# Optimization experiments

Hardware: AMD Instinct MI355X
Metric: run time of the kernel (lower is better)

The kernel has to match this reference:

```python
import jax, jax.numpy as jnp
import numpy as np
import math

EPS = 1e-5

def layernorm(x, w, b):
    mu = jnp.mean(x, axis=-1, keepdims=True)
    var = jnp.mean((x - mu) ** 2, axis=-1, keepdims=True)
    return (x - mu) / jnp.sqrt(var + EPS) * w + b

def pos_encoding(L, D):
    pos = jnp.arange(L, dtype=jnp.float32)[:, None]
    div = jnp.exp(jnp.arange(0, D, 2, dtype=jnp.float32) * (-math.log(10000.0) / D))
    pe = jnp.zeros((L, D), dtype=jnp.float32)
    pe = pe.at[:, 0::2].set(jnp.sin(pos * div))
    pe = pe.at[:, 1::2].set(jnp.cos(pos * div))
    return pe

def ssm_block(x, nw, nb, A, iw, ib, ow, ob):
    # x: [B,L,D]
    z = layernorm(x, nw, nb)
    proj = jnp.einsum('bld,ed->ble', z, iw) + ib  # [B,L,2D]
    u, g = jnp.split(proj, 2, axis=-1)
    g = jax.nn.sigmoid(g)
    u_t = jnp.swapaxes(u, 0, 1)  # [L,B,D]
    g_t = jnp.swapaxes(g, 0, 1)
    h0 = jnp.zeros(x.shape[::2], dtype=x.dtype)  # [B,D]
    def step(h, ug):
        ut, gt = ug
        h = gt * h + (1.0 - gt) * jnp.tanh(A * h + ut)
        return h, h
    _, hs = jax.lax.scan(step, h0, (u_t, g_t))  # hs: [L,B,D]
    out = jnp.einsum('lbd,ed->ble', hs, ow).swapaxes(0, 1).swapaxes(0, 1)
    out = jnp.einsum('lbd,ed->ble', hs, ow) + ob
    return x + out

def mha(x, qkv_w, qkv_b, ao_w, ao_b, nhead):
    B, L, D = x.shape
    dh = D // nhead
    qkv = jnp.einsum('bld,ed->ble', x, qkv_w) + qkv_b  # [B,L,3D]
    q, k, v = jnp.split(qkv, 3, axis=-1)
    def heads(t):
        return t.reshape(B, L, nhead, dh).transpose(0, 2, 1, 3)  # [B,H,L,dh]
    q, k, v = heads(q), heads(k), heads(v)
    scores = jnp.einsum('bhqd,bhkd->bhqk', q, k) / jnp.sqrt(jnp.asarray(dh, x.dtype))
    attn = jax.nn.softmax(scores, axis=-1)
    out = jnp.einsum('bhqk,bhkd->bhqd', attn, v)
    out = out.transpose(0, 2, 1, 3).reshape(B, L, D)
    return jnp.einsum('bld,ed->ble', out, ao_w) + ao_b

def encoder_layer(x, l1w, l1b, l2w, l2b, qkv_w, qkv_b, ao_w, ao_b, f1w, f1b, f2w, f2b, nhead):
    # norm_first pre-LN encoder layer, relu FFN, no dropout (eval)
    x = x + mha(layernorm(x, l1w, l1b), qkv_w, qkv_b, ao_w, ao_b, nhead)
    h = layernorm(x, l2w, l2b)
    h = jax.nn.relu(jnp.einsum('bld,fd->blf', h, f1w) + f1b)
    h = jnp.einsum('blf,df->bld', h, f2w) + f2b
    return x + h

def setup_inputs() -> dict:
    key = jax.random.key(0)
    ks = jax.random.split(key, 16)
    B, L, F, D, S, T = 8, 2048, 64, 128, 2, 2
    s = 0.05
    inp = {
        'x': jax.random.normal(ks[0], (B, L, F), jnp.float32),
        'in_w': jax.random.normal(ks[1], (D, F), jnp.float32) * s,
        'in_b': jnp.zeros((D,), jnp.float32),
        'ssm_norm_w': jnp.ones((S, D), jnp.float32),
        'ssm_norm_b': jnp.zeros((S, D), jnp.float32),
        'ssm_A': jax.random.normal(ks[2], (S, D), jnp.float32) * 0.1,
        'ssm_in_w': jax.random.normal(ks[3], (S, 2 * D, D), jnp.float32) * s,
        'ssm_in_b': jnp.zeros((S, 2 * D), jnp.float32),
        'ssm_out_w': jax.random.normal(ks[4], (S, D, D), jnp.float32) * s,
        'ssm_out_b': jnp.zeros((S, D), jnp.float32),
        'ln1_w': jnp.ones((T, D), jnp.float32),
        'ln1_b': jnp.zeros((T, D), jnp.float32),
        'ln2_w': jnp.ones((T, D), jnp.float32),
        'ln2_b': jnp.zeros((T, D), jnp.float32),
        'qkv_w': jax.random.normal(ks[5], (T, 3 * D, D), jnp.float32) * s,
        'qkv_b': jnp.zeros((T, 3 * D), jnp.float32),
        'ao_w': jax.random.normal(ks[6], (T, D, D), jnp.float32) * s,
        'ao_b': jnp.zeros((T, D), jnp.float32),
        'ff1_w': jax.random.normal(ks[7], (T, 4 * D, D), jnp.float32) * s,
        'ff1_b': jnp.zeros((T, 4 * D), jnp.float32),
        'ff2_w': jax.random.normal(ks[8], (T, D, 4 * D), jnp.float32) * s,
        'ff2_b': jnp.zeros((T, D), jnp.float32),
        'hln_w': jnp.ones((D,), jnp.float32),
        'hln_b': jnp.zeros((D,), jnp.float32),
        'h1_w': jax.random.normal(ks[9], (D, D), jnp.float32) * s,
        'h1_b': jnp.zeros((D,), jnp.float32),
        'h2_w': jax.random.normal(ks[10], (1, D), jnp.float32) * s,
        'h2_b': jnp.zeros((1,), jnp.float32),
    }
    return inp

NHEAD = 4

def reference(x, in_w, in_b, ssm_norm_w, ssm_norm_b, ssm_A, ssm_in_w, ssm_in_b,
              ssm_out_w, ssm_out_b, ln1_w, ln1_b, ln2_w, ln2_b, qkv_w, qkv_b,
              ao_w, ao_b, ff1_w, ff1_b, ff2_w, ff2_b, hln_w, hln_b, h1_w, h1_b,
              h2_w, h2_b):
    B, L, _ = x.shape
    D = in_w.shape[0]
    h = jnp.einsum('blf,df->bld', x, in_w) + in_b
    h = h + pos_encoding(L, D)[None]
    for i in range(ssm_A.shape[0]):
        h = ssm_block(h, ssm_norm_w[i], ssm_norm_b[i], ssm_A[i],
                      ssm_in_w[i], ssm_in_b[i], ssm_out_w[i], ssm_out_b[i])
    for i in range(ln1_w.shape[0]):
        h = encoder_layer(h, ln1_w[i], ln1_b[i], ln2_w[i], ln2_b[i],
                          qkv_w[i], qkv_b[i], ao_w[i], ao_b[i],
                          ff1_w[i], ff1_b[i], ff2_w[i], ff2_b[i], NHEAD)
    pooled = 0.5 * h[:, -1, :] + 0.5 * jnp.mean(h, axis=1)  # [B,D]
    p = layernorm(pooled, hln_w, hln_b)
    p = jax.nn.gelu(p @ h1_w.T + h1_b, approximate=False)
    return p @ h2_w.T + h2_b  # [B,1]
```

## Files before the change

kernel.cpp:

```cpp
#include <hip/hip_runtime.h>
#include <hip/hip_bf16.h>
#include <math.h>

#define L_SEQ 2048
#define D_MODEL 128
#define N_ROWS 16384
#define LOG2E 1.4426950408889634f

typedef __attribute__((ext_vector_type(8))) short bf16x8;
typedef __attribute__((ext_vector_type(4))) short short4v;
typedef __attribute__((ext_vector_type(4))) float f32x4;
typedef __attribute__((ext_vector_type(4))) unsigned uint4v;

__device__ __forceinline__ short f2bf(float x)
{
    __hip_bfloat16 b = __float2bfloat16(x);
    return *reinterpret_cast<short*>(&b);
}
__device__ __forceinline__ short f2bf_fast(float x)
{
    unsigned u = __builtin_bit_cast(unsigned, x);
    return (short)((u + 0x8000u) >> 16);
}
__device__ __forceinline__ unsigned cvt_pk_bf16(float lo, float hi)
{
    unsigned r;
    asm("v_cvt_pk_bf16_f32 %0, %1, %2" : "=v"(r) : "v"(lo), "v"(hi));
    return r;
}
__device__ __forceinline__ float bf2f(short s)
{
    unsigned u = ((unsigned)(unsigned short)s) << 16;
    return __builtin_bit_cast(float, u);
}
__device__ __forceinline__ short f2h(float x)
{
    _Float16 h = (_Float16)x;
    return (short)__builtin_bit_cast(unsigned short, h);
}
__device__ __forceinline__ float h2f(short s)
{
    _Float16 h = __builtin_bit_cast(_Float16, (unsigned short)s);
    return (float)h;
}

__global__ __launch_bounds__(256) void convert_kernel(
    const float* __restrict__ x,    const float* __restrict__ inw,
    const float* __restrict__ ssmi, const float* __restrict__ ssmo,
    const float* __restrict__ qkvw, const float* __restrict__ aow,
    const float* __restrict__ f1w,  const float* __restrict__ f2w,
    short* __restrict__ xb, short* __restrict__ wb)
{
    int it = blockIdx.x * 256 + threadIdx.x;
    const float* src; short* dst; int off;
    if      (it < 131072) { src = x;    dst = xb;          off = it; }
    else if (it < 132096) { src = inw;  dst = wb;          off = it - 131072; }
    else if (it < 140288) { src = ssmi; dst = wb + 8192;   off = it - 132096; }
    else if (it < 144384) { src = ssmo; dst = wb + 73728;  off = it - 140288; }
    else if (it < 156672) { src = qkvw; dst = wb + 106496; off = it - 144384; }
    else if (it < 160768) { src = aow;  dst = wb + 204800; off = it - 156672; }
    else if (it < 177152) { src = f1w;  dst = wb + 237568; off = it - 160768; }
    else                  { src = f2w;  dst = wb + 368640; off = it - 177152; }
    off <<= 3;
    float4 v0 = *(const float4*)(src + off);
    float4 v1 = *(const float4*)(src + off + 4);
    bf16x8 p = {f2bf(v0.x), f2bf(v0.y), f2bf(v0.z), f2bf(v0.w),
                f2bf(v1.x), f2bf(v1.y), f2bf(v1.z), f2bf(v1.w)};
    *(bf16x8*)(dst + off) = p;
}

template <int FUSE, int RED>
__global__ __launch_bounds__(256) void gemm_ln(const short* __restrict__ A,
                                               const short* __restrict__ W,
                                               const float* __restrict__ bias,
                                               const float* __restrict__ lnw,
                                               const float* __restrict__ lnb,
                                               float* __restrict__ bh,
                                               short* __restrict__ lnout,
                                               int K,
                                               const float* __restrict__ pO,
                                               const float* __restrict__ prs)
{
    __shared__ __align__(16) short As[32][72];
    __shared__ __align__(16) short Bs[128][72];
    __shared__ float2 red[2][32];

    const int tid  = threadIdx.x;
    const int wave = tid >> 6;
    const int lane = tid & 63;
    const int m    = lane & 15;
    const int quad = lane >> 4;
    const int rh   = wave & 1;
    const int ch   = wave >> 1;
    const int n0   = blockIdx.x * 32;

    const int arow = tid >> 3, acol = (tid & 7) << 3;
    const int brow = tid >> 1, bcol = (tid & 1) << 5;

    const short* Ap = A + (size_t)(n0 + arow) * K + acol;
    const short* Wp = W + (size_t)brow * K + bcol;

    f32x4 acc[4];
#pragma unroll
    for (int i = 0; i < 4; ++i) acc[i] = (f32x4){0.f, 0.f, 0.f, 0.f};

    bf16x8 a0;
    float4 ra0, ra1, rb0, rb1;
    float inva = 0.f;
    if (RED) {
        int row = n0 + arow;
        int hh  = acol >> 5;
        float rsv = prs[(size_t)hh * N_ROWS + row] + prs[(size_t)(4 + hh) * N_ROWS + row];
        inva = 1.f / rsv;
        const float* p0 = pO + (size_t)row * 128 + acol;
        const float* p1 = p0 + (size_t)N_ROWS * 128;
        ra0 = *(const float4*)p0;
        ra1 = *(const float4*)(p0 + 4);
        rb0 = *(const float4*)p1;
        rb1 = *(const float4*)(p1 + 4);
    } else {
        a0 = *(const bf16x8*)Ap;
    }
    bf16x8 b0 = *(const bf16x8*)Wp;
    bf16x8 b1 = *(const bf16x8*)(Wp + 8);
    bf16x8 b2 = *(const bf16x8*)(Wp + 16);
    bf16x8 b3 = *(const bf16x8*)(Wp + 24);

    for (int k0 = 0; k0 < K; k0 += 64) {
        if (RED) {
            uint4v pk;
            pk.x = cvt_pk_bf16((ra0.x + rb0.x) * inva, (ra0.y + rb0.y) * inva);
            pk.y = cvt_pk_bf16((ra0.z + rb0.z) * inva, (ra0.w + rb0.w) * inva);
            pk.z = cvt_pk_bf16((ra1.x + rb1.x) * inva, (ra1.y + rb1.y) * inva);
            pk.w = cvt_pk_bf16((ra1.z + rb1.z) * inva, (ra1.w + rb1.w) * inva);
            *(bf16x8*)&As[arow][acol] = __builtin_bit_cast(bf16x8, pk);
        } else {
            *(bf16x8*)&As[arow][acol] = a0;
        }
        *(bf16x8*)&Bs[brow][bcol]      = b0;
        *(bf16x8*)&Bs[brow][bcol + 8]  = b1;
        *(bf16x8*)&Bs[brow][bcol + 16] = b2;
        *(bf16x8*)&Bs[brow][bcol + 24] = b3;
        __syncthreads();
        if (k0 + 64 < K) {
            if (RED) {
                int row = n0 + arow;
                int col = k0 + 64 + acol;
                int hh  = col >> 5;
                float rsv = prs[(size_t)hh * N_ROWS + row] + prs[(size_t)(4 + hh) * N_ROWS + row];
                inva = 1.f / rsv;
                const float* p0 = pO + (size_t)row * 128 + col;
                const float* p1 = p0 + (size_t)N_ROWS * 128;
                ra0 = *(const float4*)p0;
                ra1 = *(const float4*)(p0 + 4);
                rb0 = *(const float4*)p1;
                rb1 = *(const float4*)(p1 + 4);
            } else {
                a0 = *(const bf16x8*)(Ap + k0 + 64);
            }
            b0 = *(const bf16x8*)(Wp + k0 + 64);
            b1 = *(const bf16x8*)(Wp + k0 + 72);
            b2 = *(const bf16x8*)(Wp + k0 + 80);
            b3 = *(const bf16x8*)(Wp + k0 + 88);
        }
#pragma unroll
        for (int ks = 0; ks < 2; ++ks) {
            bf16x8 af = *(const bf16x8*)&As[(rh << 4) + m][(ks << 5) + (quad << 3)];
#pragma unroll
            for (int nt = 0; nt < 4; ++nt) {
                bf16x8 bfr = *(const bf16x8*)&Bs[(ch << 6) + (nt << 4) + m][(ks << 5) + (quad << 3)];
                acc[nt] = __builtin_amdgcn_mfma_f32_16x16x32_bf16(af, bfr, acc[nt], 0, 0, 0);
            }
        }
        __syncthreads();
    }

#pragma unroll
    for (int nt = 0; nt < 4; ++nt) {
        int col = (ch << 6) + (nt << 4) + m;
        float bv = bias[col];
        float fr = 0.f;
        if (FUSE == 0)
            fr = __expf((float)(col & ~1) * (-0.07195578415606394f));
#pragma unroll
        for (int r = 0; r < 4; ++r) {
            int row = n0 + (rh << 4) + (quad << 2) + r;
            float t = acc[nt][r] + bv;
            if (FUSE == 0) {
                float ang = (float)(row & (L_SEQ - 1)) * fr;
                t += (col & 1) ? cosf(ang) : sinf(ang);
            } else {
                t += bh[(size_t)row * 128 + col];
            }
            acc[nt][r] = t;
            bh[(size_t)row * 128 + col] = t;
        }
    }

    if (FUSE < 2) {
        float wv[4], bvn[4];
#pragma unroll
        for (int nt = 0; nt < 4; ++nt) {
            wv[nt]  = lnw[(ch << 6) + (nt << 4) + m];
            bvn[nt] = lnb[(ch << 6) + (nt << 4) + m];
        }
        float s1[4], s2[4];
#pragma unroll
        for (int r = 0; r < 4; ++r) {
            float s = 0.f, q = 0.f;
#pragma unroll
            for (int nt = 0; nt < 4; ++nt) {
                float t = acc[nt][r];
                s += t;
                q = fmaf(t, t, q);
            }
            s += __shfl_xor(s, 1);  q += __shfl_xor(q, 1);
            s += __shfl_xor(s, 2);  q += __shfl_xor(q, 2);
            s += __shfl_xor(s, 4);  q += __shfl_xor(q, 4);
            s += __shfl_xor(s, 8);  q += __shfl_xor(q, 8);
            s1[r] = s; s2[r] = q;
            if (m == 0) red[ch][(rh << 4) + (quad << 2) + r] = make_float2(s, q);
        }
        __syncthreads();
#pragma unroll
        for (int r = 0; r < 4; ++r) {
            float2 o = red[ch ^ 1][(rh << 4) + (quad << 2) + r];
            float ts = s1[r] + o.x;
            float tq = s2[r] + o.y;
            float mean = ts * (1.f / 128.f);
            float var  = tq * (1.f / 128.f) - mean * mean;
            float inv  = rsqrtf(var + 1e-5f);
            int row = n0 + (rh << 4) + (quad << 2) + r;
#pragma unroll
            for (int nt = 0; nt < 4; ++nt) {
                int col = (ch << 6) + (nt << 4) + m;
                lnout[(size_t)row * 128 + col] =
                    f2bf((acc[nt][r] - mean) * inv * wv[nt] + bvn[nt]);
            }
        }
    }
}

enum { EPI_BF_RELU = 0, EPI_QKV = 1, EPI_SCAN_T = 2 };

template <int EPI>
__global__ __launch_bounds__(256) void gemm_bf(const short* __restrict__ A,
                                               const short* __restrict__ W,
                                               const float* __restrict__ bias,
                                               short* __restrict__ outb,
                                               short* __restrict__ outv,
                                               int K, int E)
{
    __shared__ __align__(16) short As[64][136];
    __shared__ __align__(16) short Bs[64][136];

    const int tid  = threadIdx.x;
    const int wave = tid >> 6;
    const int lane = tid & 63;
    const int m    = lane & 15;
    const int quad = lane >> 4;

    const int n0 = blockIdx.y * 64;
    const int e0 = blockIdx.x * 64;

    const int srow = tid >> 2;
    const int scol = (tid & 3) << 5;

    const short* Ap = A + (size_t)(n0 + srow) * K + scol;
    const short* Wp = W + (size_t)(e0 + srow) * K + scol;

    bf16x8 a0 = *(const bf16x8*)(Ap);
    bf16x8 a1 = *(const bf16x8*)(Ap + 8);
    bf16x8 a2 = *(const bf16x8*)(Ap + 16);
    bf16x8 a3 = *(const bf16x8*)(Ap + 24);
    bf16x8 w0 = *(const bf16x8*)(Wp);
    bf16x8 w1 = *(const bf16x8*)(Wp + 8);
    bf16x8 w2 = *(const bf16x8*)(Wp + 16);
    bf16x8 w3 = *(const bf16x8*)(Wp + 24);
    *(bf16x8*)&As[srow][scol]      = a0;
    *(bf16x8*)&As[srow][scol + 8]  = a1;
    *(bf16x8*)&As[srow][scol + 16] = a2;
    *(bf16x8*)&As[srow][scol + 24] = a3;
    *(bf16x8*)&Bs[srow][scol]      = w0;
    *(bf16x8*)&Bs[srow][scol + 8]  = w1;
    *(bf16x8*)&Bs[srow][scol + 16] = w2;
    *(bf16x8*)&Bs[srow][scol + 24] = w3;
    __syncthreads();

    f32x4 acc[4];
#pragma unroll
    for (int i = 0; i < 4; ++i) acc[i] = (f32x4){0.f, 0.f, 0.f, 0.f};

#pragma unroll
    for (int ks = 0; ks < 4; ++ks) {
        bf16x8 af = *(const bf16x8*)&As[(wave << 4) + m][(ks << 5) + (quad << 3)];
#pragma unroll
        for (int nt = 0; nt < 4; ++nt) {
            bf16x8 bfr = *(const bf16x8*)&Bs[(nt << 4) + m][(ks << 5) + (quad << 3)];
            acc[nt] = __builtin_amdgcn_mfma_f32_16x16x32_bf16(af, bfr, acc[nt], 0, 0, 0);
        }
    }

    if (EPI == EPI_QKV) {
        const float QSC = 0.17677669529663687f * LOG2E;
        if (e0 < 256) {
            short* dst = (e0 < 128) ? outb : (outb + 2097152);
            int cbase = (e0 < 128) ? e0 : (e0 - 128);
#pragma unroll
            for (int nt = 0; nt < 4; ++nt) {
                int col = cbase + (nt << 4) + m;
                float bv = bias[e0 + (nt << 4) + m];
#pragma unroll
                for (int r = 0; r < 4; ++r) {
                    int row = n0 + (wave << 4) + (quad << 2) + r;
                    float v = acc[nt][r] + bv;
                    if (e0 < 128) v *= QSC;
                    dst[(size_t)row * 128 + col] = f2bf(v);
                }
            }
        } else {
            int bb_ = n0 >> 11;
            int l0  = (n0 & (L_SEQ - 1)) + (wave << 4) + (quad << 2);
#pragma unroll
            for (int nt = 0; nt < 4; ++nt) {
                int c  = (e0 - 256) + (nt << 4) + m;
                int hh = c >> 5, dd = c & 31;
                float bv = bias[e0 + (nt << 4) + m];
                short4v pk;
#pragma unroll
                for (int r = 0; r < 4; ++r) pk[r] = f2bf(acc[nt][r] + bv);
                *(short4v*)&outv[(size_t)((bb_ * 4 + hh) * 32 + dd) * L_SEQ + l0] = pk;
            }
        }
    } else if (EPI == EPI_SCAN_T) {
        int bb_ = n0 >> 11;
        int l0  = (n0 & (L_SEQ - 1)) + (wave << 4) + (quad << 2);
#pragma unroll
        for (int nt = 0; nt < 4; ++nt) {
            int col = e0 + (nt << 4) + m;
            float bv = bias[col];
            short4v pk;
            if (e0 < 128) {
#pragma unroll
                for (int r = 0; r < 4; ++r)
                    pk[r] = f2h((acc[nt][r] + bv) * (2.f * LOG2E));
            } else {
#pragma unroll
                for (int r = 0; r < 4; ++r) {
                    float gr = acc[nt][r] + bv;
                    float g = __builtin_amdgcn_rcpf(
                        1.f + __builtin_amdgcn_exp2f(-gr * LOG2E));
                    pk[r] = f2h(g);
                }
            }
            *(short4v*)&outb[(((size_t)(bb_ * 256 + col)) << 11) + l0] = pk;
        }
    } else {
#pragma unroll
        for (int nt = 0; nt < 4; ++nt) {
            int col = e0 + (nt << 4) + m;
            float bv = bias[col];
#pragma unroll
            for (int r = 0; r < 4; ++r) {
                int row = n0 + (wave << 4) + (quad << 2) + r;
                float v = fmaxf(acc[nt][r] + bv, 0.f);
                outb[(size_t)row * E + col] = f2bf(v);
            }
        }
    }
}

#define SCAN_WARM 128

__device__ __forceinline__ void scan8(float& h, bf16x8 u8, bf16x8 g8,
                                      float a2, short* __restrict__ ob, int l0)
{
#pragma unroll
    for (int i = 0; i < 8; ++i) {
        float u2 = h2f(u8[i]);
        float g  = h2f(g8[i]);
        float omg = 1.f - g;
        float m2  = -2.f * omg;
        float c0 = fmaf(g, h, omg);
        float e2 = __builtin_amdgcn_exp2f(fmaf(a2, h, u2));
        float r  = __builtin_amdgcn_rcpf(1.f + e2);
        h = fmaf(m2, r, c0);
        ob[(l0 + i) * D_MODEL] = f2bf(h);
    }
}

__device__ __forceinline__ void scan8_ns(float& h, bf16x8 u8, bf16x8 g8,
                                         float a2)
{
#pragma unroll
    for (int i = 0; i < 8; ++i) {
        float u2 = h2f(u8[i]);
        float g  = h2f(g8[i]);
        float omg = 1.f - g;
        float m2  = -2.f * omg;
        float c0 = fmaf(g, h, omg);
        float e2 = __builtin_amdgcn_exp2f(fmaf(a2, h, u2));
        float r  = __builtin_amdgcn_rcpf(1.f + e2);
        h = fmaf(m2, r, c0);
    }
}

__global__ __launch_bounds__(64) void scan_kernel(const short* __restrict__ pt,
                                                  const float* __restrict__ A,
                                                  short* __restrict__ hs)
{
    int blk = blockIdx.x;
    int c   = blk & 15;
    int bd  = blk >> 4;
    int b   = bd >> 1;
    int d   = ((bd & 1) << 6) + threadIdx.x;
    float a2 = 2.f * A[d] * LOG2E;
    const short* up = pt + (((size_t)(b * 256 + d)) << 11);
    const short* gp = up + (((size_t)128) << 11);
    short* ob = hs + ((size_t)(b << 11)) * D_MODEL + d;

    const int lw = c << 7;
    float h = 0.f;

    bf16x8 uA0, uA1, gA0, gA1;

    if (c > 0) {
        int l0 = lw - SCAN_WARM;
        uA0 = *(const bf16x8*)(up + l0);
        uA1 = *(const bf16x8*)(up + l0 + 8);
        gA0 = *(const bf16x8*)(gp + l0);
        gA1 = *(const bf16x8*)(gp + l0 + 8);
        for (int l = l0; l < lw; l += 32) {
            bf16x8 uB0 = *(const bf16x8*)(up + l + 16);
            bf16x8 uB1 = *(const bf16x8*)(up + l + 24);
            bf16x8 gB0 = *(const bf16x8*)(gp + l + 16);
            bf16x8 gB1 = *(const bf16x8*)(gp + l + 24);
            scan8_ns(h, uA0, gA0, a2);
            scan8_ns(h, uA1, gA1, a2);
            uA0 = *(const bf16x8*)(up + l + 32);
            uA1 = *(const bf16x8*)(up + l + 40);
            gA0 = *(const bf16x8*)(gp + l + 32);
            gA1 = *(const bf16x8*)(gp + l + 40);
            scan8_ns(h, uB0, gB0, a2);
            scan8_ns(h, uB1, gB1, a2);
        }
    } else {
        uA0 = *(const bf16x8*)(up);
        uA1 = *(const bf16x8*)(up + 8);
        gA0 = *(const bf16x8*)(gp);
        gA1 = *(const bf16x8*)(gp + 8);
    }

    for (int l = lw; l < lw + 128; l += 32) {
        bf16x8 uB0 = *(const bf16x8*)(up + l + 16);
        bf16x8 uB1 = *(const bf16x8*)(up + l + 24);
        bf16x8 gB0 = *(const bf16x8*)(gp + l + 16);
        bf16x8 gB1 = *(const bf16x8*)(gp + l + 24);
        scan8(h, uA0, gA0, a2, ob, l);
        scan8(h, uA1, gA1, a2, ob, l + 8);
        if (l + 32 < lw + 128) {
            uA0 = *(const bf16x8*)(up + l + 32);
            uA1 = *(const bf16x8*)(up + l + 40);
            gA0 = *(const bf16x8*)(gp + l + 32);
            gA1 = *(const bf16x8*)(gp + l + 40);
        }
        scan8(h, uB0, gB0, a2, ob, l + 16);
        scan8(h, uB1, gB1, a2, ob, l + 24);
    }
}

__global__ __launch_bounds__(256) void attn_kernel(const short* __restrict__ Qs,
                                                   const short* __restrict__ Ks,
                                                   const short* __restrict__ Vtg,
                                                   float* __restrict__ pO,
                                                   float* __restrict__ prs)
{
    __shared__ __align__(16) short Klds[2][64][40];
    __shared__ __align__(16) short Vlds[2][32][72];
    __shared__ __align__(16) short Plds[4][32][68];

    const int tid  = threadIdx.x;
    const int wave = tid >> 6;
    const int lane = tid & 63;
    const int m    = lane & 15;
    const int quad = lane >> 4;

    const int raw = blockIdx.x;
    const int bid = (raw & 7) * 128 + (raw >> 3);
    const int b    = bid >> 7;
    const int h    = (bid >> 5) & 3;
    const int qh   = bid & 31;
    const int q0   = (qh >> 1) << 7;
    const int half = qh & 1;
    const int kv0  = half << 10;

    const size_t qrow = (size_t)((b << 11) + q0 + (wave << 5) + m);
    bf16x8 qfA = *(const bf16x8*)&Qs[qrow * 128 + (h << 5) + (quad << 3)];
    bf16x8 qfB = *(const bf16x8*)&Qs[(qrow + 16) * 128 + (h << 5) + (quad << 3)];

    f32x4 O00 = {0.f,0.f,0.f,0.f}, O01 = {0.f,0.f,0.f,0.f};
    f32x4 O10 = {0.f,0.f,0.f,0.f}, O11 = {0.f,0.f,0.f,0.f};
    float rs0 = 0.f, rs1 = 0.f;

    const int krow = tid >> 2, dg = (tid & 3) << 3;
    const int vrow = tid >> 3, kg = (tid & 7) << 3;
    const short* kbase = Ks + ((size_t)((b << 11) + kv0) + krow) * 128 + (h << 5) + dg;
    const short* vbase = Vtg + ((size_t)((b << 2) + h) * 32 + vrow) * L_SEQ + kv0 + kg;

    bf16x8 kreg = *(const bf16x8*)kbase;
    bf16x8 vreg = *(const bf16x8*)vbase;
    *(bf16x8*)&Klds[0][krow][dg] = kreg;
    *(bf16x8*)&Vlds[0][vrow][kg] = vreg;
    __syncthreads();

    for (int kc = 0; kc < 16; ++kc) {
        const int cur = kc & 1;
        if (kc < 15) {
            kreg = *(const bf16x8*)(kbase + (size_t)((kc + 1) << 6) * 128);
            vreg = *(const bf16x8*)(vbase + ((kc + 1) << 6));
        }

#pragma unroll
        for (int kt = 0; kt < 4; ++kt) {
            bf16x8 kf = *(const bf16x8*)&Klds[cur][(kt << 4) + m][quad << 3];
            f32x4 S0 = __builtin_amdgcn_mfma_f32_16x16x32_bf16(
                kf, qfA, (f32x4){0.f, 0.f, 0.f, 0.f}, 0, 0, 0);
            f32x4 S1 = __builtin_amdgcn_mfma_f32_16x16x32_bf16(
                kf, qfB, (f32x4){0.f, 0.f, 0.f, 0.f}, 0, 0, 0);
            float a0 = __builtin_amdgcn_exp2f(S0[0]);
            float a1 = __builtin_amdgcn_exp2f(S0[1]);
            float a2 = __builtin_amdgcn_exp2f(S0[2]);
            float a3 = __builtin_amdgcn_exp2f(S0[3]);
            rs0 += a0 + a1 + a2 + a3;
            uint2 pkA;
            pkA.x = cvt_pk_bf16(a0, a1);
            pkA.y = cvt_pk_bf16(a2, a3);
            *(uint2*)&Plds[wave][m][(kt << 4) + (quad << 2)] = pkA;
            float b0 = __builtin_amdgcn_exp2f(S1[0]);
            float b1 = __builtin_amdgcn_exp2f(S1[1]);
            float b2 = __builtin_amdgcn_exp2f(S1[2]);
            float b3 = __builtin_amdgcn_exp2f(S1[3]);
            rs1 += b0 + b1 + b2 + b3;
            uint2 pkB;
            pkB.x = cvt_pk_bf16(b0, b1);
            pkB.y = cvt_pk_bf16(b2, b3);
            *(uint2*)&Plds[wave][16 + m][(kt << 4) + (quad << 2)] = pkB;
        }

#pragma unroll
        for (int kt2 = 0; kt2 < 2; ++kt2) {
            short4v aLo = *(const short4v*)&Plds[wave][m][(kt2 << 5) + (quad << 3)];
            short4v aHi = *(const short4v*)&Plds[wave][m][(kt2 << 5) + (quad << 3) + 4];
            bf16x8 pfA = {aLo[0], aLo[1], aLo[2], aLo[3],
                          aHi[0], aHi[1], aHi[2], aHi[3]};
            short4v bLo = *(const short4v*)&Plds[wave][16 + m][(kt2 << 5) + (quad << 3)];
            short4v bHi = *(const short4v*)&Plds[wave][16 + m][(kt2 << 5) + (quad << 3) + 4];
            bf16x8 pfB = {bLo[0], bLo[1], bLo[2], bLo[3],
                          bHi[0], bHi[1], bHi[2], bHi[3]};
            bf16x8 vf0 = *(const bf16x8*)&Vlds[cur][m][(kt2 << 5) + (quad << 3)];
            bf16x8 vf1 = *(const bf16x8*)&Vlds[cur][16 + m][(kt2 << 5) + (quad << 3)];
            O00 = __builtin_amdgcn_mfma_f32_16x16x32_bf16(pfA, vf0, O00, 0, 0, 0);
            O01 = __builtin_amdgcn_mfma_f32_16x16x32_bf16(pfA, vf1, O01, 0, 0, 0);
            O10 = __builtin_amdgcn_mfma_f32_16x16x32_bf16(pfB, vf0, O10, 0, 0, 0);
            O11 = __builtin_amdgcn_mfma_f32_16x16x32_bf16(pfB, vf1, O11, 0, 0, 0);
        }

        if (kc < 15) {
            *(bf16x8*)&Klds[cur ^ 1][krow][dg] = kreg;
            *(bf16x8*)&Vlds[cur ^ 1][vrow][kg] = vreg;
        }
        __syncthreads();
    }

    rs0 += __shfl_xor(rs0, 16);
    rs0 += __shfl_xor(rs0, 32);
    rs1 += __shfl_xor(rs1, 16);
    rs1 += __shfl_xor(rs1, 32);

    const int rowbase = (b << 11) + q0 + (wave << 5);
    if (quad == 0) {
        prs[(size_t)((half << 2) + h) * N_ROWS + rowbase + m]      = rs0;
        prs[(size_t)((half << 2) + h) * N_ROWS + rowbase + 16 + m] = rs1;
    }

    float* pb = pO + (size_t)(half * N_ROWS) * 128;
#pragma unroll
    for (int r = 0; r < 4; ++r) {
        int rowA = rowbase + (quad << 2) + r;
        float* opA = pb + (size_t)rowA * 128 + (h << 5) + m;
        opA[0]  = O00[r];
        opA[16] = O01[r];
        float* opB = opA + (size_t)16 * 128;
        opB[0]  = O10[r];
        opB[16] = O11[r];
    }
}

__global__ __launch_bounds__(1024) void pool_head_kernel(
    const float* __restrict__ h,
    const float* __restrict__ hlnw, const float* __restrict__ hlnb,
    const float* __restrict__ h1w, const float* __restrict__ h1b,
    const float* __restrict__ h2w, const float* __restrict__ h2b,
    float* __restrict__ out)
{
    __shared__ float part[8][128];
    __shared__ float sd[128];
    __shared__ float sq[128];

    int b   = blockIdx.x;
    int t   = threadIdx.x;
    int d   = t & 127;
    int seg = t >> 7;
    const float* hb = h + (size_t)b * L_SEQ * D_MODEL;

    float acc = 0.f;
    int l0 = seg << 8;
    for (int l = l0; l < l0 + 256; l += 4) {
        acc += hb[(l + 0) * D_MODEL + d] + hb[(l + 1) * D_MODEL + d]
             + hb[(l + 2) * D_MODEL + d] + hb[(l + 3) * D_MODEL + d];
    }
    part[seg][d] = acc;
    __syncthreads();

    float v = 0.f;
    if (t < 128) {
        float s = 0.f;
#pragma unroll
        for (int i = 0; i < 8; ++i) s += part[i][t];
        v = 0.5f * hb[(L_SEQ - 1) * D_MODEL + t] + 0.5f * (s * (1.f / (float)L_SEQ));
        sd[t] = v;
    }
    __syncthreads();
    for (int s = 64; s > 0; s >>= 1) {
        if (t < s) sd[t] += sd[t + s];
        __syncthreads();
    }
    float mu = sd[0] * (1.f / 128.f);
    __syncthreads();
    float dv = v - mu;
    if (t < 128) sd[t] = dv * dv;
    __syncthreads();
    for (int s = 64; s > 0; s >>= 1) {
        if (t < s) sd[t] += sd[t + s];
        __syncthreads();
    }
    float var = sd[0] * (1.f / 128.f);
    __syncthreads();
    if (t < 128) sq[t] = dv * rsqrtf(var + 1e-5f) * hlnw[t] + hlnb[t];
    __syncthreads();
    if (t < 128) {
        float dot = h1b[t];
        for (int d2 = 0; d2 < 128; ++d2) dot = fmaf(sq[d2], h1w[t * 128 + d2], dot);
        float ge = 0.5f * dot * (1.f + erff(dot * 0.7071067811865475f));
        sd[t] = ge * h2w[t];
    }
    __syncthreads();
    for (int s = 64; s > 0; s >>= 1) {
        if (t < s) sd[t] += sd[t + s];
        __syncthreads();
    }
    if (t == 0) out[b] = sd[0] + h2b[0];
}

extern "C" void kernel_launch(void* const* d_in, const int* in_sizes, int n_in,
                              void* d_out, int out_size, void* d_ws, size_t ws_size,
                              hipStream_t stream)
{
    (void)in_sizes; (void)n_in; (void)out_size; (void)ws_size;
    const float* x      = (const float*)d_in[0];
    const float* in_w   = (const float*)d_in[1];
    const float* in_b   = (const float*)d_in[2];
    const float* ssm_nw = (const float*)d_in[3];
    const float* ssm_nb = (const float*)d_in[4];
    const float* ssm_A  = (const float*)d_in[5];
    const float* ssm_iw = (const float*)d_in[6];
    const float* ssm_ib = (const float*)d_in[7];
    const float* ssm_ow = (const float*)d_in[8];
    const float* ssm_ob = (const float*)d_in[9];
    const float* ln1w   = (const float*)d_in[10];
    const float* ln1b   = (const float*)d_in[11];
    const float* ln2w   = (const float*)d_in[12];
    const float* ln2b   = (const float*)d_in[13];
    const float* qkvw   = (const float*)d_in[14];
    const float* qkvb   = (const float*)d_in[15];
    const float* aow    = (const float*)d_in[16];
    const float* aob    = (const float*)d_in[17];
    const float* f1w    = (const float*)d_in[18];
    const float* f1b    = (const float*)d_in[19];
    const float* f2w    = (const float*)d_in[20];
    const float* f2b    = (const float*)d_in[21];
    const float* hlnw   = (const float*)d_in[22];
    const float* hlnb   = (const float*)d_in[23];
    const float* h1w    = (const float*)d_in[24];
    const float* h1b    = (const float*)d_in[25];
    const float* h2w    = (const float*)d_in[26];
    const float* h2b    = (const float*)d_in[27];
    float* out = (float*)d_out;

    char* wsb = (char*)d_ws;
    float* bh     = (float*)(wsb);
    short* abuf   = (short*)(wsb + 8388608);
    short* bbuf   = (short*)(wsb + 25165824);
    short* qs     = (short*)(wsb + 29360128);
    short* vt     = (short*)(wsb + 37748736);
    short* xb     = (short*)(wsb + 41943040);
    short* wb     = (short*)(wsb + 44040192);
    float* pO     = (float*)(wsb + 46137344);
    float* prs    = (float*)(wsb + 62914560);
    short* ks     = qs + 2097152;

    dim3 blk(256);

    convert_kernel<<<756, blk, 0, stream>>>(x, in_w, ssm_iw, ssm_ow, qkvw, aow, f1w, f2w, xb, wb);

    gemm_ln<0, 0><<<512, blk, 0, stream>>>(
        xb, wb, in_b, ssm_nw, ssm_nb, bh, bbuf, 64, nullptr, nullptr);

    gemm_bf<EPI_SCAN_T><<<dim3(4, 256), blk, 0, stream>>>(
        bbuf, wb + 8192, ssm_ib, abuf, nullptr, 128, 256);
    scan_kernel<<<256, 64, 0, stream>>>(abuf, ssm_A, bbuf);
    gemm_ln<1, 0><<<512, blk, 0, stream>>>(
        bbuf, wb + 73728, ssm_ob, ssm_nw + 128, ssm_nb + 128, bh, bbuf, 128, nullptr, nullptr);

    gemm_bf<EPI_SCAN_T><<<dim3(4, 256), blk, 0, stream>>>(
        bbuf, wb + 8192 + 32768, ssm_ib + 256, abuf, nullptr, 128, 256);
    scan_kernel<<<256, 64, 0, stream>>>(abuf, ssm_A + 128, bbuf);
    gemm_ln<1, 0><<<512, blk, 0, stream>>>(
        bbuf, wb + 73728 + 16384, ssm_ob + 128, ln1w, ln1b, bh, bbuf, 128, nullptr, nullptr);

    gemm_bf<EPI_QKV><<<dim3(6, 256), blk, 0, stream>>>(
        bbuf, wb + 106496, qkvb, qs, vt, 128, 384);
    attn_kernel<<<1024, blk, 0, stream>>>(qs, ks, vt, pO, prs);
    gemm_ln<1, 1><<<512, blk, 0, stream>>>(
        bbuf, wb + 204800, aob, ln2w, ln2b, bh, bbuf, 128, pO, prs);
    gemm_bf<EPI_BF_RELU><<<dim3(8, 256), blk, 0, stream>>>(
        bbuf, wb + 237568, f1b, abuf, nullptr, 128, 512);
    gemm_ln<1, 0><<<512, blk, 0, stream>>>(
        abuf, wb + 368640, f2b, ln1w + 128, ln1b + 128, bh, bbuf, 512, nullptr, nullptr);

    gemm_bf<EPI_QKV><<<dim3(6, 256), blk, 0, stream>>>(
        bbuf, wb + 106496 + 49152, qkvb + 384, qs, vt, 128, 384);
    attn_kernel<<<1024, blk, 0, stream>>>(qs, ks, vt, pO, prs);
    gemm_ln<1, 1><<<512, blk, 0, stream>>>(
        bbuf, wb + 204800 + 16384, aob + 128, ln2w + 128, ln2b + 128, bh, bbuf, 128, pO, prs);
    gemm_bf<EPI_BF_RELU><<<dim3(8, 256), blk, 0, stream>>>(
        bbuf, wb + 237568 + 65536, f1b + 512, abuf, nullptr, 128, 512);
    gemm_ln<2, 0><<<512, blk, 0, stream>>>(
        abuf, wb + 368640 + 65536, f2b + 128, nullptr, nullptr, bh, nullptr, 512, nullptr, nullptr);

    pool_head_kernel<<<8, 1024, 0, stream>>>(bh, hlnw, hlnb, h1w, h1b, h2w, h2b, out);
}
```

Measured before the change: 337.2 us.

## Fuse FFN up-projection, ReLU, down-projection and residual LayerNorm into one kernel

Replaces the two-kernel FFN (gemm_bf with ReLU writing the 512-wide hidden activation to global memory, then gemm_ln reading it back) with a single ffn_kernel. Each block keeps a 32-row tile of the hidden activation in shared memory, streams W1 and W2 in chunks through a shared buffer, and applies bias, residual add and the next LayerNorm in the epilogue. This removes the global write and read of the 16384x512 bf16 intermediate and one launch per layer. In exchange each block reloads all of W1 and W2 for only 32 rows, syncs often, and uses about 45 KB of shared memory, which may lower occupancy.

```diff
diff --git a/kernel.cpp b/kernel.cpp
--- a/kernel.cpp
+++ b/kernel.cpp
@@ -236,6 +236,180 @@
                 int col = (ch << 6) + (nt << 4) + m;
                 lnout[(size_t)row * 128 + col] =
                     f2bf((acc[nt][r] - mean) * inv * wv[nt] + bvn[nt]);
+            }
+        }
+    }
+}
+
+template <int LAST>
+__global__ __launch_bounds__(256) void ffn_kernel(
+    const short* __restrict__ A,
+    const short* __restrict__ W1,
+    const float* __restrict__ b1,
+    const short* __restrict__ W2,
+    const float* __restrict__ b2,
+    const float* __restrict__ lnw,
+    const float* __restrict__ lnb,
+    float* __restrict__ bh,
+    short* __restrict__ lnout)
+{
+    __shared__ __align__(16) short As[32][136];
+    __shared__ __align__(16) short Hs[32][520];
+    __shared__ __align__(16) short Ws[8704];
+    __shared__ float2 red[2][32];
+
+    const int tid  = threadIdx.x;
+    const int wave = tid >> 6;
+    const int lane = tid & 63;
+    const int m    = lane & 15;
+    const int quad = lane >> 4;
+    const int rh   = wave & 1;
+    const int ch   = wave >> 1;
+    const int n0   = blockIdx.x * 32;
+
+    {
+        const int arow = tid >> 3, acol = (tid & 7) << 4;
+        const short* Ap = A + (size_t)(n0 + arow) * 128 + acol;
+        bf16x8 v0 = *(const bf16x8*)Ap;
+        bf16x8 v1 = *(const bf16x8*)(Ap + 8);
+        *(bf16x8*)&As[arow][acol]     = v0;
+        *(bf16x8*)&As[arow][acol + 8] = v1;
+    }
+
+    const int wrow = tid >> 2, wcol = (tid & 3) << 5;
+
+    for (int ec = 0; ec < 8; ++ec) {
+        const short* Wp = W1 + (size_t)((ec << 6) + wrow) * 128 + wcol;
+        bf16x8 u0 = *(const bf16x8*)(Wp);
+        bf16x8 u1 = *(const bf16x8*)(Wp + 8);
+        bf16x8 u2 = *(const bf16x8*)(Wp + 16);
+        bf16x8 u3 = *(const bf16x8*)(Wp + 24);
+        short* wl = &Ws[wrow * 136 + wcol];
+        *(bf16x8*)(wl)      = u0;
+        *(bf16x8*)(wl + 8)  = u1;
+        *(bf16x8*)(wl + 16) = u2;
+        *(bf16x8*)(wl + 24) = u3;
+        __syncthreads();
+
+        f32x4 acc[2];
+        acc[0] = (f32x4){0.f, 0.f, 0.f, 0.f};
+        acc[1] = (f32x4){0.f, 0.f, 0.f, 0.f};
+#pragma unroll
+        for (int ks = 0; ks < 4; ++ks) {
+            bf16x8 af = *(const bf16x8*)&As[(rh << 4) + m][(ks << 5) + (quad << 3)];
+#pragma unroll
+            for (int nt = 0; nt < 2; ++nt) {
+                bf16x8 bfr = *(const bf16x8*)&Ws[((ch << 5) + (nt << 4) + m) * 136
+                                                 + (ks << 5) + (quad << 3)];
+                acc[nt] = __builtin_amdgcn_mfma_f32_16x16x32_bf16(af, bfr, acc[nt], 0, 0, 0);
+            }
+        }
+#pragma unroll
+        for (int nt = 0; nt < 2; ++nt) {
+            int col = (ec << 6) + (ch << 5) + (nt << 4) + m;
+            float bv = b1[col];
+#pragma unroll
+            for (int r = 0; r < 4; ++r) {
+                int row = (rh << 4) + (quad << 2) + r;
+                Hs[row][col] = f2bf(fmaxf(acc[nt][r] + bv, 0.f));
+            }
+        }
+        __syncthreads();
+    }
+
+    f32x4 acc2[4];
+#pragma unroll
+    for (int i = 0; i < 4; ++i) acc2[i] = (f32x4){0.f, 0.f, 0.f, 0.f};
+
+    const int w2col = tid >> 1, w2k = (tid & 1) << 5;
+    for (int kc = 0; kc < 8; ++kc) {
+        const short* Wp2 = W2 + (size_t)w2col * 512 + (kc << 6) + w2k;
+        bf16x8 u0 = *(const bf16x8*)(Wp2);
+        bf16x8 u1 = *(const bf16x8*)(Wp2 + 8);
+        bf16x8 u2 = *(const bf16x8*)(Wp2 + 16);
+        bf16x8 u3 = *(const bf16x8*)(Wp2 + 24);
+        short* wl = &Ws[w2col * 68 + w2k];
+        uint4 t0 = __builtin_bit_cast(uint4, u0);
+        uint4 t1 = __builtin_bit_cast(uint4, u1);
+        uint4 t2 = __builtin_bit_cast(uint4, u2);
+        uint4 t3 = __builtin_bit_cast(uint4, u3);
+        *(uint2*)(wl)      = make_uint2(t0.x, t0.y);
+        *(uint2*)(wl + 4)  = make_uint2(t0.z, t0.w);
+        *(uint2*)(wl + 8)  = make_uint2(t1.x, t1.y);
+        *(uint2*)(wl + 12) = make_uint2(t1.z, t1.w);
+        *(uint2*)(wl + 16) = make_uint2(t2.x, t2.y);
+        *(uint2*)(wl + 20) = make_uint2(t2.z, t2.w);
+        *(uint2*)(wl + 24) = make_uint2(t3.x, t3.y);
+        *(uint2*)(wl + 28) = make_uint2(t3.z, t3.w);
+        __syncthreads();
+#pragma unroll
+        for (int ks = 0; ks < 2; ++ks) {
+            bf16x8 af = *(const bf16x8*)&Hs[(rh << 4) + m][(kc << 6) + (ks << 5) + (quad << 3)];
+#pragma unroll
+            for (int nt = 0; nt < 4; ++nt) {
+                const short* bp = &Ws[((ch << 6) + (nt << 4) + m) * 68 + (ks << 5) + (quad << 3)];
+                uint2 lo = *(const uint2*)bp;
+                uint2 hi = *(const uint2*)(bp + 4);
+                uint4 c; c.x = lo.x; c.y = lo.y; c.z = hi.x; c.w = hi.y;
+                bf16x8 bfr = __builtin_bit_cast(bf16x8, c);
+                acc2[nt] = __builtin_amdgcn_mfma_f32_16x16x32_bf16(af, bfr, acc2[nt], 0, 0, 0);
+            }
+        }
+        __syncthreads();
+    }
+
+#pragma unroll
+    for (int nt = 0; nt < 4; ++nt) {
+        int col = (ch << 6) + (nt << 4) + m;
+        float bv = b2[col];
+#pragma unroll
+        for (int r = 0; r < 4; ++r) {
+            int row = n0 + (rh << 4) + (quad << 2) + r;
+            float t = acc2[nt][r] + bv + bh[(size_t)row * 128 + col];
+            acc2[nt][r] = t;
+            bh[(size_t)row * 128 + col] = t;
+        }
+    }
+
+    if (!LAST) {
+        float wv[4], bvn[4];
+#pragma unroll
+        for (int nt = 0; nt < 4; ++nt) {
+            wv[nt]  = lnw[(ch << 6) + (nt << 4) + m];
+            bvn[nt] = lnb[(ch << 6) + (nt << 4) + m];
+        }
+        float s1[4], s2[4];
+#pragma unroll
+        for (int r = 0; r < 4; ++r) {
+            float s = 0.f, q = 0.f;
+#pragma unroll
+            for (int nt = 0; nt < 4; ++nt) {
+                float t = acc2[nt][r];
+                s += t;
+                q = fmaf(t, t, q);
+            }
+            s += __shfl_xor(s, 1);  q += __shfl_xor(q, 1);
+            s += __shfl_xor(s, 2);  q += __shfl_xor(q, 2);
+            s += __shfl_xor(s, 4);  q += __shfl_xor(q, 4);
+            s += __shfl_xor(s, 8);  q += __shfl_xor(q, 8);
+            s1[r] = s; s2[r] = q;
+            if (m == 0) red[ch][(rh << 4) + (quad << 2) + r] = make_float2(s, q);
+        }
+        __syncthreads();
+#pragma unroll
+        for (int r = 0; r < 4; ++r) {
+            float2 o = red[ch ^ 1][(rh << 4) + (quad << 2) + r];
+            float ts = s1[r] + o.x;
+            float tq = s2[r] + o.y;
+            float mean = ts * (1.f / 128.f);
+            float var  = tq * (1.f / 128.f) - mean * mean;
+            float inv  = rsqrtf(var + 1e-5f);
+            int row = n0 + (rh << 4) + (quad << 2) + r;
+#pragma unroll
+            for (int nt = 0; nt < 4; ++nt) {
+                int col = (ch << 6) + (nt << 4) + m;
+                lnout[(size_t)row * 128 + col] =
+                    f2bf((acc2[nt][r] - mean) * inv * wv[nt] + bvn[nt]);
             }
         }
     }
@@ -733,20 +907,17 @@
     attn_kernel<<<1024, blk, 0, stream>>>(qs, ks, vt, pO, prs);
     gemm_ln<1, 1><<<512, blk, 0, stream>>>(
         bbuf, wb + 204800, aob, ln2w, ln2b, bh, bbuf, 128, pO, prs);
-    gemm_bf<EPI_BF_RELU><<<dim3(8, 256), blk, 0, stream>>>(
-        bbuf, wb + 237568, f1b, abuf, nullptr, 128, 512);
-    gemm_ln<1, 0><<<512, blk, 0, stream>>>(
-        abuf, wb + 368640, f2b, ln1w + 128, ln1b + 128, bh, bbuf, 512, nullptr, nullptr);
+    ffn_kernel<0><<<512, blk, 0, stream>>>(
+        bbuf, wb + 237568, f1b, wb + 368640, f2b, ln1w + 128, ln1b + 128, bh, bbuf);
 
     gemm_bf<EPI_QKV><<<dim3(6, 256), blk, 0, stream>>>(
         bbuf, wb + 106496 + 49152, qkvb + 384, qs, vt, 128, 384);
     attn_kernel<<<1024, blk, 0, stream>>>(qs, ks, vt, pO, prs);
     gemm_ln<1, 1><<<512, blk, 0, stream>>>(
         bbuf, wb + 204800 + 16384, aob + 128, ln2w + 128, ln2b + 128, bh, bbuf, 128, pO, prs);
-    gemm_bf<EPI_BF_RELU><<<dim3(8, 256), blk, 0, stream>>>(
-        bbuf, wb + 237568 + 65536, f1b + 512, abuf, nullptr, 128, 512);
-    gemm_ln<2, 0><<<512, blk, 0, stream>>>(
-        abuf, wb + 368640 + 65536, f2b + 128, nullptr, nullptr, bh, nullptr, 512, nullptr, nullptr);
+    ffn_kernel<1><<<512, blk, 0, stream>>>(
+        bbuf, wb + 237568 + 65536, f1b + 512, wb + 368640 + 65536, f2b + 128,
+        nullptr, nullptr, bh, nullptr);
 
     pool_head_kernel<<<8, 1024, 0, stream>>>(bh, hlnw, hlnb, h1w, h1b, h2w, h2b, out);
 }
```

Measured after the change: 340.3 us. About the same (+0.9%).
